# Performance work log

Measured on AMD Instinct MI355X. Metric: run time of the kernel, lower is better.

The kernel has to match this reference:

```python
import jax, jax.numpy as jnp
import numpy as np

N_EMBD = 2048
HIDDEN = 2 * N_EMBD        # 4096
ADAPT = HIDDEN // 16       # 256
B, S = 4, 2048


def _layernorm(x, g, b, eps=1e-5):
    mu = jnp.mean(x, axis=-1, keepdims=True)
    var = jnp.var(x, axis=-1, keepdims=True)
    return (x - mu) * jax.lax.rsqrt(var + eps) * g + b


def setup_inputs() -> dict:
    key = jax.random.key(0)
    ks = jax.random.split(key, 7)
    scale = 1.0 / np.sqrt(N_EMBD)
    adapt_scale = scale * 0.01
    return {
        "x": jax.random.normal(ks[0], (B, S, N_EMBD), dtype=jnp.float32),
        "W_up": jax.random.normal(ks[1], (HIDDEN, N_EMBD), dtype=jnp.float32) * scale,
        "W_gate": jax.random.normal(ks[2], (HIDDEN, N_EMBD), dtype=jnp.float32) * scale,
        "W_down": jax.random.normal(ks[3], (N_EMBD, HIDDEN), dtype=jnp.float32) * scale,
        "W_pre": jax.random.normal(ks[4], (ADAPT, N_EMBD), dtype=jnp.float32) * adapt_scale,
        "W_post": jax.random.normal(ks[5], (ADAPT, HIDDEN), dtype=jnp.float32) * adapt_scale,
        "W_proj": jax.random.normal(ks[6], (HIDDEN, ADAPT), dtype=jnp.float32) * adapt_scale,
        "ln_g": jnp.ones((ADAPT,), dtype=jnp.float32),
        "ln_b": jnp.zeros((ADAPT,), dtype=jnp.float32),
    }


def reference(x, W_up, W_gate, W_down, W_pre, W_post, W_proj, ln_g, ln_b):
    # SwiGLU trunk
    up = jnp.einsum('bsd,hd->bsh', x, W_up)
    gate = jnp.einsum('bsd,hd->bsh', x, W_gate)
    hidden = jax.nn.silu(gate) * up                      # [B,S,H]
    # Low-rank quadratic adapter
    adapt_in = _layernorm(jnp.einsum('bsd,ad->bsa', x, W_pre), ln_g, ln_b)       # [B,S,A]
    adapt_out = _layernorm(jnp.einsum('bsh,ah->bsa', hidden, W_post), ln_g, ln_b)  # [B,S,A]
    aw = jnp.einsum('bsa,bta->bst', adapt_in, adapt_out)  # [B,S,S]
    aw = jax.nn.silu(jnp.clip(aw, -5.0, 5.0))
    adapt = jnp.einsum('bst,bta->bsa', aw, adapt_in)      # [B,S,A]
    adapt = 0.1 * jnp.einsum('bsa,ha->bsh', adapt, W_proj)
    hidden = hidden + adapt
    out = jnp.einsum('bsh,dh->bsd', hidden, W_down)       # dropout p=0 -> identity
    return out
```

## Files before the change

### kernel.cpp

```cpp
#include <hip/hip_runtime.h>
#include <cstdint>
#include <cstddef>

typedef unsigned short u16;
typedef short short8 __attribute__((ext_vector_type(8)));
typedef float f32x4 __attribute__((ext_vector_type(4)));

__device__ __forceinline__ u16 f2bf(float f) {
  union { float f; unsigned u; } x; x.f = f;
  unsigned r = x.u + 0x7FFFu + ((x.u >> 16) & 1u);
  return (u16)(r >> 16);
}
__device__ __forceinline__ float b2f(u16 h) {
  union { unsigned u; float f; } x; x.u = ((unsigned)h) << 16;
  return x.f;
}
__device__ __forceinline__ float silu_f(float v) {
  return v / (1.f + __expf(-v));
}
__device__ __forceinline__ void gll(const u16* g, u16* l) {
  __builtin_amdgcn_global_load_lds((const __attribute__((address_space(1))) unsigned*)g,
                                   (__attribute__((address_space(3))) unsigned*)l, 16, 0, 0);
}
__device__ __forceinline__ short8 ld8(const u16* p) { return *(const short8*)p; }

__global__ __launch_bounds__(256) void cvt7_k(const float4* __restrict__ s0,
                                              const float4* __restrict__ s1,
                                              const float4* __restrict__ s2,
                                              const float4* __restrict__ s3,
                                              const float4* __restrict__ s4,
                                              const float4* __restrict__ s5,
                                              ushort4* __restrict__ dst) {
  const int i = blockIdx.x * 256 + threadIdx.x;
  const int o1 = 4194304, o2 = 6291456, o3 = 8388608, o4 = 10485760,
            o5 = 10616832, o6 = 10878976;
  if (i >= o6) return;
  const float4* src;
  int base;
  if      (i < o1) { src = s0; base = 0;  }
  else if (i < o2) { src = s1; base = o1; }
  else if (i < o3) { src = s2; base = o2; }
  else if (i < o4) { src = s3; base = o3; }
  else if (i < o5) { src = s4; base = o4; }
  else             { src = s5; base = o5; }
  float4 v = src[i - base];
  ushort4 o;
  o.x = f2bf(v.x); o.y = f2bf(v.y); o.z = f2bf(v.z); o.w = f2bf(v.w);
  dst[i] = o;
}

__global__ __launch_bounds__(256) void tcvt_k(const float* __restrict__ in,
                                              u16* __restrict__ out) {
  __shared__ float t[64][65];
  const int h0 = blockIdx.x * 64, a0 = blockIdx.y * 64;
  const int c = threadIdx.x & 63, g = threadIdx.x >> 6;
#pragma unroll
  for (int i = 0; i < 16; ++i) {
    int r = g * 16 + i;
    t[r][c] = in[(size_t)(h0 + r) * 256 + a0 + c];
  }
  __syncthreads();
#pragma unroll
  for (int i = 0; i < 16; ++i) {
    int a = g * 16 + i;
    out[(size_t)(a0 + a) * 4096 + h0 + c] = f2bf(t[c][a]);
  }
}

__global__ __launch_bounds__(256) void red_ln_k(const float* __restrict__ part,
                                                const float* __restrict__ g,
                                                const float* __restrict__ b,
                                                u16* __restrict__ out,
                                                u16* __restrict__ outT, int Mtot) {
  const int row = blockIdx.x;
  const int a = threadIdx.x;
  const size_t stride = (size_t)Mtot * 256;
  const size_t base = (size_t)row * 256 + a;
  float v = part[base] + part[base + stride] + part[base + 2 * stride] + part[base + 3 * stride];
  float s = v, s2 = v * v;
#pragma unroll
  for (int o = 32; o; o >>= 1) { s += __shfl_down(s, o, 64); s2 += __shfl_down(s2, o, 64); }
  __shared__ float red[8];
  int l = a & 63, w = a >> 6;
  if (l == 0) { red[w] = s; red[4 + w] = s2; }
  __syncthreads();
  s  = red[0] + red[1] + red[2] + red[3];
  s2 = red[4] + red[5] + red[6] + red[7];
  float mu  = s * 0.00390625f;
  float var = s2 * 0.00390625f - mu * mu;
  float rs  = rsqrtf(var + 1e-5f);
  float o   = (v - mu) * rs * g[a] + b[a];
  u16 ob = f2bf(o);
  out[base] = ob;
  if (outT) {
    int bi = row >> 11, t = row & 2047;
    outT[((size_t)bi * 256 + a) * 2048 + t] = ob;
  }
}

template <int SK>
__global__ __launch_bounds__(256) void red_k(const float* __restrict__ part,
                                             u16* __restrict__ out, int Mtot, float scale) {
  const int row = blockIdx.x;
  const int a = threadIdx.x;
  const size_t stride = (size_t)Mtot * 256;
  const size_t base = (size_t)row * 256 + a;
  float v = 0.f;
#pragma unroll
  for (int s = 0; s < SK; ++s) v += part[base + (size_t)s * stride];
  out[base] = f2bf(v * scale);
}

template <int SK>
__global__ __launch_bounds__(256) void gemm_sk(const u16* __restrict__ A,
                                               const u16* __restrict__ B,
                                               float* __restrict__ part,
                                               int M, int N, int Kfull, int Kc,
                                               long bA, long bB, int Mtot) {
  const int z  = blockIdx.z;
  const int b  = z / SK, sk = z % SK;
  const int brow = blockIdx.y * 128;
  const int bcol = blockIdx.x * 128;
  A += (size_t)b * bA + (size_t)sk * Kc;
  B += (size_t)b * bB + (size_t)sk * Kc;

  __shared__ u16 Al[128 * 64];
  __shared__ u16 Bl[128 * 64];
  const int tid  = threadIdx.x;
  const int lane = tid & 63;
  const int w = tid >> 6, wr = w >> 1, wc = w & 1;
  const int srow = tid >> 3;
  const int scol = (((tid & 7) ^ (srow & 7)) * 8);
  const int fr   = lane & 15;
  const int kg   = lane >> 4;

  f32x4 acc[4][4] = {};

  for (int kt = 0; kt < Kc; kt += 64) {
#pragma unroll
    for (int i = 0; i < 4; ++i)
      gll(A + (size_t)(brow + i * 32 + srow) * Kfull + kt + scol, &Al[(i * 256 + tid) * 8]);
#pragma unroll
    for (int i = 0; i < 4; ++i)
      gll(B + (size_t)(bcol + i * 32 + srow) * Kfull + kt + scol, &Bl[(i * 256 + tid) * 8]);
    __syncthreads();
#pragma unroll
    for (int kk = 0; kk < 2; ++kk) {
      short8 af[4], bfr[4];
      const int ko8 = kk * 4 + kg;
#pragma unroll
      for (int m = 0; m < 4; ++m) {
        const int r = wr * 64 + m * 16 + fr;
        af[m] = ld8(&Al[r * 64 + ((ko8 ^ (fr & 7)) << 3)]);
      }
#pragma unroll
      for (int n = 0; n < 4; ++n) {
        const int r = wc * 64 + n * 16 + fr;
        bfr[n] = ld8(&Bl[r * 64 + ((ko8 ^ (fr & 7)) << 3)]);
      }
#pragma unroll
      for (int m = 0; m < 4; ++m)
#pragma unroll
        for (int n = 0; n < 4; ++n)
          acc[m][n] = __builtin_amdgcn_mfma_f32_16x16x32_bf16(af[m], bfr[n], acc[m][n], 0, 0, 0);
    }
    __syncthreads();
  }

  const int col0 = bcol + wc * 64 + fr;
  const int row0 = brow + wr * 64 + (kg << 2);
  float* P = part + ((size_t)sk * Mtot + (size_t)b * M) * N;
#pragma unroll
  for (int m = 0; m < 4; ++m)
#pragma unroll
    for (int j = 0; j < 4; ++j) {
      size_t roff = (size_t)(row0 + m * 16 + j) * N + col0;
#pragma unroll
      for (int n = 0; n < 4; ++n) P[roff + n * 16] = acc[m][n][j];
    }
}

__device__ __forceinline__ void pipe256(const u16* Abase, const u16* Bbase, int K,
                                        u16* As, u16* Bs, int tid, int wm, int wn,
                                        int lane, f32x4 (*acc)[4], int bHalfOff) {
  const int fr  = lane & 15;
  const int cs0 = ((((lane >> 4) << 4) ^ ((lane & 7) << 4)) >> 1);
  const int cs1 = cs0 ^ 32;
  const int NT = K >> 6;

  auto stageA = [&](int tt, int half) {
    const u16* s = Abase + (size_t)(half * 128) * K + (tt << 6);
    u16* d = &As[((tt & 1) * 2 + half) * 8192 + tid * 8];
    gll(s, d); gll(s + (size_t)64 * K, d + 4096);
  };
  auto stageB = [&](int tt, int half) {
    const u16* s = Bbase + (size_t)half * bHalfOff * K + (tt << 6);
    u16* d = &Bs[((tt & 1) * 2 + half) * 8192 + tid * 8];
    gll(s, d); gll(s + (size_t)64 * K, d + 4096);
  };

  stageA(0, 0); stageB(0, 0); stageA(0, 1); stageB(0, 1);
  if (NT > 1) {
    stageA(1, 0); stageB(1, 0); stageA(1, 1);
    asm volatile("s_waitcnt vmcnt(6)" ::: "memory");
  } else {
    asm volatile("s_waitcnt vmcnt(0)" ::: "memory");
  }
  __builtin_amdgcn_s_barrier();

  const int aoff0 = (wm * 64 + fr) * 64;
  const int boff0 = (wn * 32 + fr) * 64;

  short8 aLo[8], aHi[8], bb[4];

  for (int t = 0; t < NT; ++t) {
    const u16* h0a = &As[(t & 1) * 16384];
    const u16* h0b = &Bs[(t & 1) * 16384];
    const u16* h1a = h0a + 8192;
    const u16* h1b = h0b + 8192;
    const bool pf2 = (t + 2 < NT);

#pragma unroll
    for (int m = 0; m < 4; ++m) {
      aLo[m * 2]     = ld8(h0a + aoff0 + m * 1024 + cs0);
      aLo[m * 2 + 1] = ld8(h0a + aoff0 + m * 1024 + cs1);
    }
#pragma unroll
    for (int n = 0; n < 2; ++n) {
      bb[n * 2]     = ld8(h0b + boff0 + n * 1024 + cs0);
      bb[n * 2 + 1] = ld8(h0b + boff0 + n * 1024 + cs1);
    }
    if (t + 1 < NT) stageB(t + 1, 1);
    __builtin_amdgcn_s_setprio(1);
#pragma unroll
    for (int m = 0; m < 4; ++m)
#pragma unroll
      for (int n = 0; n < 2; ++n) {
        acc[m][n] = __builtin_amdgcn_mfma_f32_16x16x32_bf16(aLo[m*2],   bb[n*2],   acc[m][n], 0, 0, 0);
        acc[m][n] = __builtin_amdgcn_mfma_f32_16x16x32_bf16(aLo[m*2+1], bb[n*2+1], acc[m][n], 0, 0, 0);
      }
    __builtin_amdgcn_s_setprio(0);
    __builtin_amdgcn_s_barrier();

#pragma unroll
    for (int m = 0; m < 4; ++m) {
      aHi[m * 2]     = ld8(h1a + aoff0 + m * 1024 + cs0);
      aHi[m * 2 + 1] = ld8(h1a + aoff0 + m * 1024 + cs1);
    }
    if (pf2) { stageA(t + 2, 0); stageB(t + 2, 0); }
    __builtin_amdgcn_s_setprio(1);
#pragma unroll
    for (int m = 0; m < 4; ++m)
#pragma unroll
      for (int n = 0; n < 2; ++n) {
        acc[4+m][n] = __builtin_amdgcn_mfma_f32_16x16x32_bf16(aHi[m*2],   bb[n*2],   acc[4+m][n], 0, 0, 0);
        acc[4+m][n] = __builtin_amdgcn_mfma_f32_16x16x32_bf16(aHi[m*2+1], bb[n*2+1], acc[4+m][n], 0, 0, 0);
      }
    __builtin_amdgcn_s_setprio(0);
    if (pf2)             { asm volatile("s_waitcnt vmcnt(12)" ::: "memory"); }
    else if (t + 1 < NT) { asm volatile("s_waitcnt vmcnt(8)"  ::: "memory"); }
    else                 { asm volatile("s_waitcnt vmcnt(0)"  ::: "memory"); }
    __builtin_amdgcn_s_barrier();

#pragma unroll
    for (int n = 0; n < 2; ++n) {
      bb[n * 2]     = ld8(h1b + boff0 + n * 1024 + cs0);
      bb[n * 2 + 1] = ld8(h1b + boff0 + n * 1024 + cs1);
    }
    if (pf2) stageA(t + 2, 1);
    __builtin_amdgcn_s_setprio(1);
#pragma unroll
    for (int m = 0; m < 4; ++m)
#pragma unroll
      for (int n = 0; n < 2; ++n) {
        acc[m][2+n] = __builtin_amdgcn_mfma_f32_16x16x32_bf16(aLo[m*2],   bb[n*2],   acc[m][2+n], 0, 0, 0);
        acc[m][2+n] = __builtin_amdgcn_mfma_f32_16x16x32_bf16(aLo[m*2+1], bb[n*2+1], acc[m][2+n], 0, 0, 0);
      }
#pragma unroll
    for (int m = 0; m < 4; ++m)
#pragma unroll
      for (int n = 0; n < 2; ++n) {
        acc[4+m][2+n] = __builtin_amdgcn_mfma_f32_16x16x32_bf16(aHi[m*2],   bb[n*2],   acc[4+m][2+n], 0, 0, 0);
        acc[4+m][2+n] = __builtin_amdgcn_mfma_f32_16x16x32_bf16(aHi[m*2+1], bb[n*2+1], acc[4+m][2+n], 0, 0, 0);
      }
    __builtin_amdgcn_s_setprio(0);
    if (pf2)              { asm volatile("s_waitcnt vmcnt(8)" ::: "memory"); }
    else if (t + 1 < NT)  { asm volatile("s_waitcnt vmcnt(0)" ::: "memory"); }
    __builtin_amdgcn_s_barrier();
  }
}

template <int EPI>
__global__ __launch_bounds__(512, 2) void gemm256(const u16* __restrict__ A,
                                                  const u16* __restrict__ B,
                                                  void* __restrict__ Cv,
                                                  int N, int K,
                                                  const u16* __restrict__ A2,
                                                  const u16* __restrict__ B2, int K2,
                                                  long bA, long bB, long bC) {
  __shared__ __align__(16) u16 As[32768];
  __shared__ __align__(16) u16 Bs[32768];
  const int tid = threadIdx.x;
  const int bz  = blockIdx.z;
  A += (size_t)bz * bA;
  B += (size_t)bz * bB;

  const int gx = gridDim.x;
  const int nwg = gx * gridDim.y;
  int orig = blockIdx.y * gx + blockIdx.x;
  {
    int q = nwg >> 3, r = nwg & 7;
    int xcd = orig & 7, idx = orig >> 3;
    orig = (xcd < r) ? xcd * (q + 1) + idx : r * (q + 1) + (xcd - r) * q + idx;
  }
  const int brow = (orig / gx) * 256;
  const int bcol = (orig % gx) * ((EPI == 5) ? 128 : 256);
  const int bHalfOff = (EPI == 5) ? 4096 : 128;

  const int lane = tid & 63;
  const int wid  = tid >> 6;
  const int wm = wid >> 2, wn = wid & 3;
  const int srow = tid >> 3;
  const int scol = ((((tid & 7) << 4) ^ ((srow & 7) << 4)) >> 1);

  f32x4 acc[8][4] = {};

  pipe256(A + (size_t)(brow + srow) * K + scol,
          B + (size_t)(bcol + srow) * K + scol, K, As, Bs, tid, wm, wn, lane, acc, bHalfOff);
  if (K2 > 0)
    pipe256(A2 + (size_t)(brow + srow) * K2 + scol,
            B2 + (size_t)(bcol + srow) * K2 + scol, K2, As, Bs, tid, wm, wn, lane, acc, 128);

  const int fr = lane & 15;
  if (EPI == 0 || EPI == 2) {
#pragma unroll
    for (int m = 0; m < 8; ++m) {
      const int mrow = (m < 4) ? (wm * 64 + m * 16) : (128 + wm * 64 + (m - 4) * 16);
#pragma unroll
      for (int j = 0; j < 4; ++j) {
        const size_t roff = (size_t)(brow + mrow + ((lane >> 4) << 2) + j) * N + bcol + fr;
#pragma unroll
        for (int n = 0; n < 4; ++n) {
          const int ncol = (n < 2) ? (wn * 32 + n * 16) : (128 + wn * 32 + (n - 2) * 16);
          if (EPI == 0) {
            ((float*)Cv + (size_t)bz * bC)[roff + ncol] = acc[m][n][j];
          } else {
            float v = acc[m][n][j];
            v = fminf(5.f, fmaxf(-5.f, v));
            ((u16*)Cv + (size_t)bz * bC)[roff + ncol] = f2bf(silu_f(v));
          }
        }
      }
    }
  } else {
    u16* Cb = (u16*)Cv;
#pragma unroll
    for (int m = 0; m < 8; ++m) {
      const int mrow = (m < 4) ? (wm * 64 + m * 16) : (128 + wm * 64 + (m - 4) * 16);
#pragma unroll
      for (int j = 0; j < 4; ++j) {
        const size_t roff = (size_t)(brow + mrow + ((lane >> 4) << 2) + j) * N + bcol + wn * 32 + fr;
#pragma unroll
        for (int n = 0; n < 2; ++n)
          Cb[roff + n * 16] = f2bf(silu_f(acc[m][n + 2][j]) * acc[m][n][j]);
      }
    }
  }
}

extern "C" void kernel_launch(void* const* d_in, const int* in_sizes, int n_in,
                              void* d_out, int out_size, void* d_ws, size_t ws_size,
                              hipStream_t stream) {
  const float* x      = (const float*)d_in[0];
  const float* W_up   = (const float*)d_in[1];
  const float* W_gate = (const float*)d_in[2];
  const float* W_down = (const float*)d_in[3];
  const float* W_pre  = (const float*)d_in[4];
  const float* W_post = (const float*)d_in[5];
  const float* W_proj = (const float*)d_in[6];
  const float* ln_g   = (const float*)d_in[7];
  const float* ln_b   = (const float*)d_in[8];
  (void)in_sizes; (void)n_in; (void)out_size; (void)ws_size;

  const int D = 2048, Hh = 4096, A_ = 256, Bn = 4, S = 2048, M = 8192;

  char* p = (char*)d_ws;
  u16* xb      = (u16*)p; p += (size_t)M * D * 2;
  u16* Wug_b   = (u16*)p; p += (size_t)2 * Hh * D * 2;
  u16* Wdown_b = (u16*)p; p += (size_t)D * Hh * 2;
  u16* Wpre_b  = (u16*)p; p += (size_t)A_ * D * 2;
  u16* Wpost_b = (u16*)p; p += (size_t)A_ * Hh * 2;
  u16* WprojT  = (u16*)p; p += (size_t)Hh * A_ * 2;
  u16* hidden  = (u16*)p; p += (size_t)M * Hh * 2;
  u16* scratch = (u16*)p; p += (size_t)M * Hh * 2;
  char* q = (char*)scratch;
  u16*   aw        = (u16*)q; q += (size_t)Bn * S * S * 2;
  u16*   adapt_in  = (u16*)q; q += (size_t)M * A_ * 2;
  u16*   adapt_inT = (u16*)q; q += (size_t)M * A_ * 2;
  u16*   adapt_out = (u16*)q; q += (size_t)M * A_ * 2;
  u16*   adaptb    = (u16*)q; q += (size_t)M * A_ * 2;
  u16*   Wdp_b     = (u16*)q; q += (size_t)2048 * 256 * 2;
  float* part     = (float*)Wug_b;
  float* wdp_part = (float*)hidden;

  cvt7_k<<<dim3(42496), dim3(256), 0, stream>>>((const float4*)x, (const float4*)W_up,
                                                (const float4*)W_gate, (const float4*)W_down,
                                                (const float4*)W_pre, (const float4*)W_post,
                                                (ushort4*)xb);
  tcvt_k<<<dim3(64, 4), dim3(256), 0, stream>>>(W_proj, WprojT);

  gemm_sk<8><<<dim3(A_ / 128, 2048 / 128, 8), 256, 0, stream>>>(Wdown_b, WprojT, wdp_part,
                                                                2048, A_, Hh, Hh / 8, 0, 0, 2048);
  red_k<8><<<dim3(2048), 256, 0, stream>>>(wdp_part, Wdp_b, 2048, 0.1f);

  gemm256<5><<<dim3(Hh / 128, M / 256), 512, 0, stream>>>(xb, Wug_b, hidden,
                                                          Hh, D, nullptr, nullptr, 0, 0, 0, 0);

  gemm_sk<4><<<dim3(A_ / 128, M / 128, 4), 256, 0, stream>>>(xb, Wpre_b, part,
                                                             M, A_, D, D / 4, 0, 0, M);
  red_ln_k<<<dim3(M), 256, 0, stream>>>(part, ln_g, ln_b, adapt_in, adapt_inT, M);

  gemm_sk<4><<<dim3(A_ / 128, M / 128, 4), 256, 0, stream>>>(hidden, Wpost_b, part,
                                                             M, A_, Hh, Hh / 4, 0, 0, M);
  red_ln_k<<<dim3(M), 256, 0, stream>>>(part, ln_g, ln_b, adapt_out, nullptr, M);

  gemm256<2><<<dim3(S / 256, S / 256, Bn), 512, 0, stream>>>(adapt_in, adapt_out, aw,
                                                             S, A_, nullptr, nullptr, 0,
                                                             (long)S * A_, (long)S * A_,
                                                             (long)S * S);

  gemm_sk<4><<<dim3(A_ / 128, S / 128, Bn * 4), 256, 0, stream>>>(aw, adapt_inT, part,
                                                                  S, A_, S, S / 4,
                                                                  (long)S * S, (long)A_ * S, M);
  red_k<4><<<dim3(M), 256, 0, stream>>>(part, adaptb, M, 1.0f);

  gemm256<0><<<dim3(D / 256, M / 256), 512, 0, stream>>>(hidden, Wdown_b, d_out,
                                                         D, Hh, adaptb, Wdp_b, A_, 0, 0, 0);
}
```

Baseline: 560.8 us.

## Replace 256x256 GEMM pipeline with K=32 triple-buffered single-phase loop

Rewrites the main GEMM inner pipeline from a double-buffered K=64 step split into three barrier-separated phases into a K=32 step with three LDS buffers and a single barrier per iteration. Tile staging now loads 4 rows-by-32 columns per thread with a new XOR swizzle, and LDS per block shrinks from 128KB to 96KB. The goal is to cut barrier count and phase overhead and allow deeper prefetch, at the cost of twice as many iterations and fewer MFMAs per barrier.

```diff
diff --git a/kernel.cpp b/kernel.cpp
--- a/kernel.cpp
+++ b/kernel.cpp
@@ -180,112 +180,58 @@
     }
 }
 
-__device__ __forceinline__ void pipe256(const u16* Abase, const u16* Bbase, int K,
-                                        u16* As, u16* Bs, int tid, int wm, int wn,
-                                        int lane, f32x4 (*acc)[4], int bHalfOff) {
-  const int fr  = lane & 15;
-  const int cs0 = ((((lane >> 4) << 4) ^ ((lane & 7) << 4)) >> 1);
-  const int cs1 = cs0 ^ 32;
-  const int NT = K >> 6;
-
-  auto stageA = [&](int tt, int half) {
-    const u16* s = Abase + (size_t)(half * 128) * K + (tt << 6);
-    u16* d = &As[((tt & 1) * 2 + half) * 8192 + tid * 8];
-    gll(s, d); gll(s + (size_t)64 * K, d + 4096);
+__device__ __forceinline__ void pipe32(const u16* Asrc, const u16* Bsrc, int K,
+                                       u16* As, u16* Bs, int tid, int wm, int wn,
+                                       int lane, f32x4 (*acc)[4], size_t bOff2) {
+  const int NT = K >> 5;
+
+  auto stage = [&](int tt) {
+    const int b = tt % 3;
+    const u16* sa = Asrc + (tt << 5);
+    const u16* sb = Bsrc + (tt << 5);
+    u16* da = &As[b * 8192 + tid * 8];
+    u16* db = &Bs[b * 8192 + tid * 8];
+    gll(sa, da); gll(sa + (size_t)128 * K, da + 4096);
+    gll(sb, db); gll(sb + bOff2, db + 4096);
   };
-  auto stageB = [&](int tt, int half) {
-    const u16* s = Bbase + (size_t)half * bHalfOff * K + (tt << 6);
-    u16* d = &Bs[((tt & 1) * 2 + half) * 8192 + tid * 8];
-    gll(s, d); gll(s + (size_t)64 * K, d + 4096);
-  };
-
-  stageA(0, 0); stageB(0, 0); stageA(0, 1); stageB(0, 1);
+
+  stage(0);
   if (NT > 1) {
-    stageA(1, 0); stageB(1, 0); stageA(1, 1);
-    asm volatile("s_waitcnt vmcnt(6)" ::: "memory");
+    stage(1);
+    asm volatile("s_waitcnt vmcnt(4)" ::: "memory");
   } else {
     asm volatile("s_waitcnt vmcnt(0)" ::: "memory");
   }
   __builtin_amdgcn_s_barrier();
 
-  const int aoff0 = (wm * 64 + fr) * 64;
-  const int boff0 = (wn * 32 + fr) * 64;
-
-  short8 aLo[8], aHi[8], bb[4];
+  const int rb = (lane & 15) * 32 + ((((lane >> 4) ^ ((lane >> 1) & 3))) << 3);
+  short8 af[8], bf2[4];
 
   for (int t = 0; t < NT; ++t) {
-    const u16* h0a = &As[(t & 1) * 16384];
-    const u16* h0b = &Bs[(t & 1) * 16384];
-    const u16* h1a = h0a + 8192;
-    const u16* h1b = h0b + 8192;
-    const bool pf2 = (t + 2 < NT);
-
-#pragma unroll
-    for (int m = 0; m < 4; ++m) {
-      aLo[m * 2]     = ld8(h0a + aoff0 + m * 1024 + cs0);
-      aLo[m * 2 + 1] = ld8(h0a + aoff0 + m * 1024 + cs1);
-    }
-#pragma unroll
-    for (int n = 0; n < 2; ++n) {
-      bb[n * 2]     = ld8(h0b + boff0 + n * 1024 + cs0);
-      bb[n * 2 + 1] = ld8(h0b + boff0 + n * 1024 + cs1);
-    }
-    if (t + 1 < NT) stageB(t + 1, 1);
+    const int cb = t % 3;
+    const u16* aB = &As[cb * 8192];
+    const u16* bB = &Bs[cb * 8192];
+
+#pragma unroll
+    for (int n = 0; n < 4; ++n) {
+      const int off = (n < 2) ? (wn * 1024 + n * 512) : (4096 + wn * 1024 + (n - 2) * 512);
+      bf2[n] = ld8(bB + off + rb);
+    }
+#pragma unroll
+    for (int m = 0; m < 8; ++m) {
+      const int off = (m < 4) ? (wm * 2048 + m * 512) : (4096 + wm * 2048 + (m - 4) * 512);
+      af[m] = ld8(aB + off + rb);
+    }
+    if (t + 2 < NT) stage(t + 2);
     __builtin_amdgcn_s_setprio(1);
 #pragma unroll
-    for (int m = 0; m < 4; ++m)
-#pragma unroll
-      for (int n = 0; n < 2; ++n) {
-        acc[m][n] = __builtin_amdgcn_mfma_f32_16x16x32_bf16(aLo[m*2],   bb[n*2],   acc[m][n], 0, 0, 0);
-        acc[m][n] = __builtin_amdgcn_mfma_f32_16x16x32_bf16(aLo[m*2+1], bb[n*2+1], acc[m][n], 0, 0, 0);
-      }
+    for (int m = 0; m < 8; ++m)
+#pragma unroll
+      for (int n = 0; n < 4; ++n)
+        acc[m][n] = __builtin_amdgcn_mfma_f32_16x16x32_bf16(af[m], bf2[n], acc[m][n], 0, 0, 0);
     __builtin_amdgcn_s_setprio(0);
-    __builtin_amdgcn_s_barrier();
-
-#pragma unroll
-    for (int m = 0; m < 4; ++m) {
-      aHi[m * 2]     = ld8(h1a + aoff0 + m * 1024 + cs0);
-      aHi[m * 2 + 1] = ld8(h1a + aoff0 + m * 1024 + cs1);
-    }
-    if (pf2) { stageA(t + 2, 0); stageB(t + 2, 0); }
-    __builtin_amdgcn_s_setprio(1);
-#pragma unroll
-    for (int m = 0; m < 4; ++m)
-#pragma unroll
-      for (int n = 0; n < 2; ++n) {
-        acc[4+m][n] = __builtin_amdgcn_mfma_f32_16x16x32_bf16(aHi[m*2],   bb[n*2],   acc[4+m][n], 0, 0, 0);
-        acc[4+m][n] = __builtin_amdgcn_mfma_f32_16x16x32_bf16(aHi[m*2+1], bb[n*2+1], acc[4+m][n], 0, 0, 0);
-      }
-    __builtin_amdgcn_s_setprio(0);
-    if (pf2)             { asm volatile("s_waitcnt vmcnt(12)" ::: "memory"); }
-    else if (t + 1 < NT) { asm volatile("s_waitcnt vmcnt(8)"  ::: "memory"); }
-    else                 { asm volatile("s_waitcnt vmcnt(0)"  ::: "memory"); }
-    __builtin_amdgcn_s_barrier();
-
-#pragma unroll
-    for (int n = 0; n < 2; ++n) {
-      bb[n * 2]     = ld8(h1b + boff0 + n * 1024 + cs0);
-      bb[n * 2 + 1] = ld8(h1b + boff0 + n * 1024 + cs1);
-    }
-    if (pf2) stageA(t + 2, 1);
-    __builtin_amdgcn_s_setprio(1);
-#pragma unroll
-    for (int m = 0; m < 4; ++m)
-#pragma unroll
-      for (int n = 0; n < 2; ++n) {
-        acc[m][2+n] = __builtin_amdgcn_mfma_f32_16x16x32_bf16(aLo[m*2],   bb[n*2],   acc[m][2+n], 0, 0, 0);
-        acc[m][2+n] = __builtin_amdgcn_mfma_f32_16x16x32_bf16(aLo[m*2+1], bb[n*2+1], acc[m][2+n], 0, 0, 0);
-      }
-#pragma unroll
-    for (int m = 0; m < 4; ++m)
-#pragma unroll
-      for (int n = 0; n < 2; ++n) {
-        acc[4+m][2+n] = __builtin_amdgcn_mfma_f32_16x16x32_bf16(aHi[m*2],   bb[n*2],   acc[4+m][2+n], 0, 0, 0);
-        acc[4+m][2+n] = __builtin_amdgcn_mfma_f32_16x16x32_bf16(aHi[m*2+1], bb[n*2+1], acc[4+m][2+n], 0, 0, 0);
-      }
-    __builtin_amdgcn_s_setprio(0);
-    if (pf2)              { asm volatile("s_waitcnt vmcnt(8)" ::: "memory"); }
-    else if (t + 1 < NT)  { asm volatile("s_waitcnt vmcnt(0)" ::: "memory"); }
+    if (t + 2 < NT)      { asm volatile("s_waitcnt vmcnt(4)" ::: "memory"); }
+    else if (t + 1 < NT) { asm volatile("s_waitcnt vmcnt(0)" ::: "memory"); }
     __builtin_amdgcn_s_barrier();
   }
 }
@@ -298,8 +244,8 @@
                                                   const u16* __restrict__ A2,
                                                   const u16* __restrict__ B2, int K2,
                                                   long bA, long bB, long bC) {
-  __shared__ __align__(16) u16 As[32768];
-  __shared__ __align__(16) u16 Bs[32768];
+  __shared__ __align__(16) u16 As[24576];
+  __shared__ __align__(16) u16 Bs[24576];
   const int tid = threadIdx.x;
   const int bz  = blockIdx.z;
   A += (size_t)bz * bA;
@@ -320,16 +266,18 @@
   const int lane = tid & 63;
   const int wid  = tid >> 6;
   const int wm = wid >> 2, wn = wid & 3;
-  const int srow = tid >> 3;
-  const int scol = ((((tid & 7) << 4) ^ ((srow & 7) << 4)) >> 1);
+  const int srow2 = tid >> 2;
+  const int scol2 = ((tid & 3) ^ ((tid >> 3) & 3)) << 3;
 
   f32x4 acc[8][4] = {};
 
-  pipe256(A + (size_t)(brow + srow) * K + scol,
-          B + (size_t)(bcol + srow) * K + scol, K, As, Bs, tid, wm, wn, lane, acc, bHalfOff);
+  pipe32(A + (size_t)(brow + srow2) * K + scol2,
+         B + (size_t)(bcol + srow2) * K + scol2, K, As, Bs, tid, wm, wn, lane, acc,
+         (size_t)bHalfOff * K);
   if (K2 > 0)
-    pipe256(A2 + (size_t)(brow + srow) * K2 + scol,
-            B2 + (size_t)(bcol + srow) * K2 + scol, K2, As, Bs, tid, wm, wn, lane, acc, 128);
+    pipe32(A2 + (size_t)(brow + srow2) * K2 + scol2,
+           B2 + (size_t)(bcol + srow2) * K2 + scol2, K2, As, Bs, tid, wm, wn, lane, acc,
+           (size_t)128 * K2);
 
   const int fr = lane & 15;
   if (EPI == 0 || EPI == 2) {
```

Result: slower. 587.7 us (+4.8%).
